# Kernel tuning notes

Hardware: AMD Instinct MI355X
Metric: run time of the kernel (lower is better)

Reference implementation:

```python
import jax, jax.numpy as jnp
import numpy as np

EPS = 0.001  # numerical_stabilizer


def setup_inputs() -> dict:
    key = jax.random.key(0)
    ks = jax.random.split(key, 8)
    B, L, D, H, M = 4, 4096, 1024, 16, 64
    scale = 0.02
    return {
        "query": jax.random.normal(ks[0], (B, L, D), jnp.float32),
        "key": jax.random.normal(ks[1], (B, L, D), jnp.float32),
        "value": jax.random.normal(ks[2], (B, L, D), jnp.float32),
        "Wq": jax.random.normal(ks[3], (D, H, M), jnp.float32) * scale,
        "bq": jnp.zeros((H, M), jnp.float32),
        "Wk": jax.random.normal(ks[4], (D, H, M), jnp.float32) * scale,
        "bk": jnp.zeros((H, M), jnp.float32),
        "Wv": jax.random.normal(ks[5], (D, H, M), jnp.float32) * scale,
        "bv": jnp.zeros((H, M), jnp.float32),
        "Wo": jax.random.normal(ks[6], (H, M, D), jnp.float32) * scale,
        "bo": jnp.zeros((D,), jnp.float32),
        "step": 0,
    }


def reference(query, key, value, Wq, bq, Wk, bk, Wv, bv, Wo, bo, step):
    # QKV projections: [B,L,D] x [D,H,M] -> [B,L,H,M]
    q = jnp.einsum('bld,dhm->blhm', query, Wq) + bq
    k = jnp.einsum('bld,dhm->blhm', key, Wk) + bk
    v = jnp.einsum('bld,dhm->blhm', value, Wv) + bv
    # ReLU feature map with stabilizer
    q = jax.nn.relu(q) + EPS
    k = jax.nn.relu(k) + EPS
    # Linear (kernelized) attention: KV outer-product state [B,H,M,M]
    kvs = jnp.einsum('blhm,blhd->bhmd', k, v)
    a_v = jnp.einsum('blhm,bhmd->blhd', q, kvs)
    # Normalizer: sum of keys over sequence
    ks_sum = jnp.sum(k, axis=1)                       # [B,H,M]
    norm = jnp.einsum('blhm,bhm->blh', q, ks_sum)     # [B,L,H]
    a_v = a_v / norm[..., None]
    # Output projection over (head, head_dim) -> hidden
    out = jnp.einsum('blhm,hmd->bld', a_v, Wo) + bo
    return out
```

## Files before the change

kernel.cpp:

```cpp
#include <hip/hip_runtime.h>
#include <stdint.h>


typedef __bf16 bf16;
typedef __bf16 bf16x4 __attribute__((ext_vector_type(4)));
typedef __bf16 bf16x8 __attribute__((ext_vector_type(8)));
typedef float f32x4 __attribute__((ext_vector_type(4)));

#define MFMA_(a, b, c) __builtin_amdgcn_mfma_f32_16x16x32_bf16((a), (b), (c), 0, 0, 0)

static constexpr int BB   = 4;
static constexpr int LSEQ = 4096;
static constexpr int DIM  = 1024;
static constexpr int HH   = 16;
static constexpr float EPSF = 0.001f;

__device__ __forceinline__ void gload16(bf16* lds, const bf16* g) {
  __builtin_amdgcn_global_load_lds(
      (const __attribute__((address_space(1))) void*)g,
      (__attribute__((address_space(3))) void*)lds, 16, 0, 0);
}

__global__ void k_cvt(const float* __restrict__ q, const float* __restrict__ k,
                      const float* __restrict__ v, bf16* __restrict__ xb) {
  const int nchunk = 3 << 21;
  const int stride = gridDim.x * blockDim.x;
  for (int c = blockIdx.x * blockDim.x + threadIdx.x; c < nchunk; c += stride) {
    const int t = c >> 21;
    const size_t off = (size_t)(c & ((1 << 21) - 1)) * 8;
    const float* src = (t == 0) ? q : (t == 1) ? k : v;
    const f32x4* sp = reinterpret_cast<const f32x4*>(src + off);
    const f32x4 a = __builtin_nontemporal_load(sp);
    const f32x4 b = __builtin_nontemporal_load(sp + 1);
    bf16x8 o;
    o[0] = (bf16)a[0]; o[1] = (bf16)a[1]; o[2] = (bf16)a[2]; o[3] = (bf16)a[3];
    o[4] = (bf16)b[0]; o[5] = (bf16)b[1]; o[6] = (bf16)b[2]; o[7] = (bf16)b[3];
    *reinterpret_cast<bf16x8*>(xb + (size_t)t * 16777216u + off) = o;
  }
}

__global__ void k_prep_w4(const float* __restrict__ W0, const float* __restrict__ W1,
                          const float* __restrict__ W2, const float* __restrict__ W3,
                          bf16* __restrict__ T0, bf16* __restrict__ T1,
                          bf16* __restrict__ T2, bf16* __restrict__ T3) {
  const float* W; bf16* T;
  switch (blockIdx.z) {
    case 0:  W = W0; T = T0; break;
    case 1:  W = W1; T = T1; break;
    case 2:  W = W2; T = T2; break;
    default: W = W3; T = T3; break;
  }
  __shared__ float t[32][33];
  const int tx = threadIdx.x & 31, ty = threadIdx.x >> 5;
  const int r0 = blockIdx.x * 32, c0 = blockIdx.y * 32;
#pragma unroll
  for (int j = 0; j < 32; j += 8)
    t[ty + j][tx] = W[(size_t)(r0 + ty + j) * DIM + c0 + tx];
  __syncthreads();
#pragma unroll
  for (int j = 0; j < 32; j += 8)
    T[(size_t)(c0 + ty + j) * DIM + r0 + tx] = (bf16)t[tx][ty + j];
}

__global__ void k_init_vt(bf16* __restrict__ vt) {
  const int c = blockIdx.x * 256 + threadIdx.x;
  const int l8 = c & 511;
  const int r  = (c >> 9) & 15;
  const int bh = c >> 13;
  const bf16 val = (r == 0) ? (bf16)1.0f : (bf16)0.0f;
  bf16x8 o;
#pragma unroll
  for (int j = 0; j < 8; ++j) o[j] = val;
  *reinterpret_cast<bf16x8*>(vt + ((size_t)bh * 80 + 64 + r) * LSEQ + l8 * 8) = o;
}

__device__ __forceinline__ void stage_half(bf16 (&As)[2][16384], bf16 (&Bs)[2][16384],
                                           const bf16* Ab, const bf16* Bb,
                                           int h, int w, int srow, int scol) {
  const int t = h >> 2, reg = h & 3, buf = t & 1;
  bf16* lds = (reg < 2) ? &As[buf][(reg & 1) * 8192] : &Bs[buf][(reg & 1) * 8192];
  const bf16* g = (reg < 2) ? Ab : Bb;
  const int rbase = (reg & 1) * 128;
#pragma unroll
  for (int rr = 0; rr < 2; ++rr) {
    const int row = rbase + (rr * 8 + w) * 8 + srow;
    gload16(lds + (rr * 8 + w) * 512, g + (size_t)row * DIM + t * 64 + scol);
  }
}

#define LDA(d, g, f)                                                                              \
  a[d][0] = *reinterpret_cast<const bf16x8*>(&As[g][(wm * 128 + (f) * 16 + lr) * 64 + col0]);     \
  a[d][1] = *reinterpret_cast<const bf16x8*>(&As[g][(wm * 128 + (f) * 16 + lr) * 64 + col1]);
#define LDB(d, g, c)                                                                              \
  b[d][0] = *reinterpret_cast<const bf16x8*>(&Bs[g][(wn * 64 + (c) * 16 + lr) * 64 + col0]);      \
  b[d][1] = *reinterpret_cast<const bf16x8*>(&Bs[g][(wn * 64 + (c) * 16 + lr) * 64 + col1]);
#define MM(fi, ci, fo, co)                                                                        \
  acc[fo][co] = MFMA_(a[fi][0], b[ci][0], acc[fo][co]);                                           \
  acc[fo][co] = MFMA_(a[fi][1], b[ci][1], acc[fo][co]);

#define PHASE(g, q, pidx)                                                                         \
  {                                                                                               \
    if ((q) == 0) { LDA(0, g, 0) LDA(1, g, 1) LDA(2, g, 2) LDA(3, g, 3)                           \
                    LDB(0, g, 0) LDB(1, g, 1) }                                                   \
    else if ((q) == 1) { LDB(0, g, 2) LDB(1, g, 3) }                                              \
    else if ((q) == 2) { LDA(0, g, 4) LDA(1, g, 5) LDA(2, g, 6) LDA(3, g, 7) }                    \
    else { LDB(0, g, 0) LDB(1, g, 1) }                                                            \
    const int hh = 8 * i + 5 + (pidx);                                                            \
    if (hh < 64) stage_half(As, Bs, Ab, Bb, hh, w, srow, scol);                                   \
    if ((pidx) == 3 || (pidx) == 7) {                                                             \
      if (i < 7) { asm volatile("s_waitcnt vmcnt(2)" ::: "memory"); }                             \
      else       { asm volatile("s_waitcnt vmcnt(0)" ::: "memory"); }                             \
    }                                                                                             \
    __builtin_amdgcn_sched_barrier(0);                                                            \
    __builtin_amdgcn_s_barrier();                                                                 \
    __builtin_amdgcn_sched_barrier(0);                                                            \
    __builtin_amdgcn_s_setprio(1);                                                                \
    if ((q) == 0) { MM(0, 0, 0, 0) MM(1, 0, 1, 0) MM(2, 0, 2, 0) MM(3, 0, 3, 0)                   \
                    MM(0, 1, 0, 1) MM(1, 1, 1, 1) MM(2, 1, 2, 1) MM(3, 1, 3, 1) }                 \
    else if ((q) == 1) { MM(0, 0, 0, 2) MM(1, 0, 1, 2) MM(2, 0, 2, 2) MM(3, 0, 3, 2)              \
                         MM(0, 1, 0, 3) MM(1, 1, 1, 3) MM(2, 1, 2, 3) MM(3, 1, 3, 3) }            \
    else if ((q) == 2) { MM(0, 0, 4, 2) MM(1, 0, 5, 2) MM(2, 0, 6, 2) MM(3, 0, 7, 2)              \
                         MM(0, 1, 4, 3) MM(1, 1, 5, 3) MM(2, 1, 6, 3) MM(3, 1, 7, 3) }            \
    else { MM(0, 0, 4, 0) MM(1, 0, 5, 0) MM(2, 0, 6, 0) MM(3, 0, 7, 0)                            \
           MM(0, 1, 4, 1) MM(1, 1, 5, 1) MM(2, 1, 6, 1) MM(3, 1, 7, 1) }                          \
    __builtin_amdgcn_s_setprio(0);                                                                \
    __builtin_amdgcn_sched_barrier(0);                                                            \
    __builtin_amdgcn_s_barrier();                                                                 \
    __builtin_amdgcn_sched_barrier(0);                                                            \
  }

template <int MODE>
__global__ __launch_bounds__(512, 2) void k_gemm256(const bf16* __restrict__ X,
                                                    const bf16* __restrict__ WT,
                                                    const float* __restrict__ bias,
                                                    void* __restrict__ outp) {
  __shared__ __align__(16) bf16 As[2][16384];
  __shared__ __align__(16) bf16 Bs[2][16384];
  const int tid = threadIdx.x;
  const int lane = tid & 63, w = tid >> 6;
  const int wm = w >> 2, wn = w & 3;
  const int lr = lane & 15, lk = (lane >> 4) & 3;
  const int n0 = blockIdx.x * 256, c0 = blockIdx.y * 256;
  const int swz = (lr & 7) * 8;
  const int col0 = (lk * 8) ^ swz;
  const int col1 = (lk * 8 + 32) ^ swz;
  const int srow = lane >> 3;
  const int scol = (((lane & 7) ^ ((lane >> 3) & 7)) * 8);
  const bf16* Ab = X + (size_t)n0 * DIM;
  const bf16* Bb = WT + (size_t)c0 * DIM;

  f32x4 acc[8][4] = {};
  bf16x8 a[4][2], b[2][2];

#pragma unroll
  for (int h = 0; h < 5; ++h) stage_half(As, Bs, Ab, Bb, h, w, srow, scol);
  asm volatile("s_waitcnt vmcnt(2)" ::: "memory");
  __builtin_amdgcn_sched_barrier(0);
  __builtin_amdgcn_s_barrier();
  __builtin_amdgcn_sched_barrier(0);

  for (int i = 0; i < 8; ++i) {
    PHASE(0, 0, 0) PHASE(0, 1, 1) PHASE(0, 2, 2) PHASE(0, 3, 3)
    PHASE(1, 0, 4) PHASE(1, 1, 5) PHASE(1, 2, 6) PHASE(1, 3, 7)
  }

  float bvv[4];
#pragma unroll
  for (int cb = 0; cb < 4; ++cb) bvv[cb] = bias[c0 + wn * 64 + cb * 16 + lr];
  const int bidx = n0 >> 12;
  const int l0 = n0 & (LSEQ - 1);
#pragma unroll
  for (int f = 0; f < 8; ++f) {
#pragma unroll
    for (int cb = 0; cb < 4; ++cb) {
      const int c = c0 + wn * 64 + cb * 16 + lr;
      if (MODE == 0) {
        bf16* out = (bf16*)outp;
#pragma unroll
        for (int r = 0; r < 4; ++r) {
          float x = acc[f][cb][r] + bvv[cb];
          x = fmaxf(x, 0.f) + EPSF;
          const int row = n0 + wm * 128 + f * 16 + lk * 4 + r;
          out[(size_t)row * DIM + c] = (bf16)x;
        }
      } else if (MODE == 3) {
        float* out = (float*)outp;
#pragma unroll
        for (int r = 0; r < 4; ++r) {
          const int row = n0 + wm * 128 + f * 16 + lk * 4 + r;
          out[(size_t)row * DIM + c] = acc[f][cb][r] + bvv[cb];
        }
      } else {
        bf16* out = (bf16*)outp;
        const int l = l0 + wm * 128 + f * 16 + lk * 4;
        bf16x4 o;
#pragma unroll
        for (int r = 0; r < 4; ++r) {
          float x = acc[f][cb][r] + bvv[cb];
          if (MODE == 1) x = fmaxf(x, 0.f) + EPSF;
          o[r] = (bf16)x;
        }
        size_t rowbase;
        if (MODE == 1) rowbase = (size_t)bidx * 1024 + c;
        else           rowbase = ((size_t)(bidx * HH + (c >> 6)) * 80 + (c & 63));
        *reinterpret_cast<bf16x4*>(out + rowbase * LSEQ + l) = o;
      }
    }
  }
}
#undef PHASE
#undef MM
#undef LDB
#undef LDA

__global__ __launch_bounds__(256, 2) void k_kvs(const bf16* __restrict__ kt,
                                                const bf16* __restrict__ vt,
                                                float* __restrict__ kvs) {
  const int tid = threadIdx.x, lane = tid & 63, wid = tid >> 6;
  const int lr = lane & 15, lk = lane >> 4;
  const int bh = blockIdx.y;
  const int lbase = blockIdx.x * 512;
  __shared__ bf16 As[64][64];
  __shared__ bf16 Bs[80][64];
  f32x4 acc[5] = {};
  const bf16* ktb = kt + (size_t)bh * 64 * LSEQ;
  const bf16* vtb = vt + (size_t)bh * 80 * LSEQ;

  for (int ks = 0; ks < 8; ++ks) {
    const int l0 = lbase + ks * 64;
    __syncthreads();
#pragma unroll
    for (int i = 0; i < 2; ++i) {
      const int e = i * 2048 + tid * 8;
      const int row = e >> 6, col = e & 63;
      *reinterpret_cast<bf16x8*>(&As[row][col]) =
          *reinterpret_cast<const bf16x8*>(ktb + (size_t)row * LSEQ + l0 + col);
    }
#pragma unroll
    for (int i = 0; i < 2; ++i) {
      const int e = i * 2048 + tid * 8;
      const int row = e >> 6, col = e & 63;
      *reinterpret_cast<bf16x8*>(&Bs[row][col]) =
          *reinterpret_cast<const bf16x8*>(vtb + (size_t)row * LSEQ + l0 + col);
    }
    if (tid < 128) {
      const int e = 4096 + tid * 8;
      const int row = e >> 6, col = e & 63;
      *reinterpret_cast<bf16x8*>(&Bs[row][col]) =
          *reinterpret_cast<const bf16x8*>(vtb + (size_t)row * LSEQ + l0 + col);
    }
    __syncthreads();
#pragma unroll
    for (int kk = 0; kk < 2; ++kk) {
      const bf16x8 af = *reinterpret_cast<const bf16x8*>(&As[wid * 16 + lr][kk * 32 + lk * 8]);
#pragma unroll
      for (int cb = 0; cb < 5; ++cb) {
        const bf16x8 bfr = *reinterpret_cast<const bf16x8*>(&Bs[cb * 16 + lr][kk * 32 + lk * 8]);
        acc[cb] = MFMA_(af, bfr, acc[cb]);
      }
    }
  }
  float* kb = kvs + (size_t)bh * 64 * 80;
#pragma unroll
  for (int cb = 0; cb < 5; ++cb) {
    const int dcol = cb * 16 + lr;
#pragma unroll
    for (int r = 0; r < 4; ++r) {
      const int m = wid * 16 + lk * 4 + r;
      atomicAdd(kb + m * 80 + dcol, acc[cb][r]);
    }
  }
}

__global__ void k_kvs_t(const float* __restrict__ kvs, bf16* __restrict__ bav) {
  const int bh = blockIdx.x;
  const float* src = kvs + (size_t)bh * 5120;
  bf16* dst = bav + (size_t)bh * 5120;
  for (int i = threadIdx.x; i < 5120; i += 256) {
    const int dp = i >> 6, mm = i & 63;
    dst[i] = (bf16)src[mm * 80 + dp];
  }
}

__global__ __launch_bounds__(256, 2) void k_av(const bf16* __restrict__ q,
                                               const bf16* __restrict__ bav,
                                               bf16* __restrict__ avn) {
  const int tid = threadIdx.x, lane = tid & 63, wid = tid >> 6;
  const int lr = lane & 15, lk = lane >> 4;
  const int bh = blockIdx.y, b = bh >> 4, h = bh & 15;
  const int l0 = blockIdx.x * 128;
  __shared__ bf16 As[128][64];
  __shared__ bf16 Bs[80][64];
  __shared__ float nrm[128];

  const bf16* qb = q + ((size_t)b * LSEQ + l0) * DIM + h * 64;
#pragma unroll
  for (int i = 0; i < 4; ++i) {
    const int e = i * 2048 + tid * 8;
    const int row = e >> 6, col = e & 63;
    *reinterpret_cast<bf16x8*>(&As[row][col]) =
        *reinterpret_cast<const bf16x8*>(qb + (size_t)row * DIM + col);
  }
  const bf16* bb = bav + (size_t)bh * 5120;
#pragma unroll
  for (int i = 0; i < 2; ++i) {
    const int e = i * 2048 + tid * 8;
    const int row = e >> 6, col = e & 63;
    *reinterpret_cast<bf16x8*>(&Bs[row][col]) =
        *reinterpret_cast<const bf16x8*>(bb + row * 64 + col);
  }
  if (tid < 128) {
    const int e = 4096 + tid * 8;
    const int row = e >> 6, col = e & 63;
    *reinterpret_cast<bf16x8*>(&Bs[row][col]) =
        *reinterpret_cast<const bf16x8*>(bb + row * 64 + col);
  }
  __syncthreads();

  f32x4 acc[2][5] = {};
#pragma unroll
  for (int kk = 0; kk < 2; ++kk) {
    bf16x8 af[2];
    af[0] = *reinterpret_cast<const bf16x8*>(&As[wid * 32 + lr][kk * 32 + lk * 8]);
    af[1] = *reinterpret_cast<const bf16x8*>(&As[wid * 32 + 16 + lr][kk * 32 + lk * 8]);
#pragma unroll
    for (int cb = 0; cb < 5; ++cb) {
      const bf16x8 bfr = *reinterpret_cast<const bf16x8*>(&Bs[cb * 16 + lr][kk * 32 + lk * 8]);
      acc[0][cb] = MFMA_(af[0], bfr, acc[0][cb]);
      acc[1][cb] = MFMA_(af[1], bfr, acc[1][cb]);
    }
  }
  if (lr == 0) {
#pragma unroll
    for (int rb = 0; rb < 2; ++rb)
#pragma unroll
      for (int r = 0; r < 4; ++r)
        nrm[wid * 32 + rb * 16 + lk * 4 + r] = acc[rb][4][r];
  }
  __syncthreads();
  bf16* ob = avn + ((size_t)b * LSEQ + l0) * DIM + h * 64;
#pragma unroll
  for (int rb = 0; rb < 2; ++rb) {
#pragma unroll
    for (int cb = 0; cb < 4; ++cb) {
#pragma unroll
      for (int r = 0; r < 4; ++r) {
        const int row = wid * 32 + rb * 16 + lk * 4 + r;
        const float x = acc[rb][cb][r] / nrm[row];
        ob[(size_t)row * DIM + cb * 16 + lr] = (bf16)x;
      }
    }
  }
}

extern "C" void kernel_launch(void* const* d_in, const int* in_sizes, int n_in,
                              void* d_out, int out_size, void* d_ws, size_t ws_size,
                              hipStream_t stream) {
  const float* query = (const float*)d_in[0];
  const float* key   = (const float*)d_in[1];
  const float* value = (const float*)d_in[2];
  const float* Wq    = (const float*)d_in[3];
  const float* bq    = (const float*)d_in[4];
  const float* Wk    = (const float*)d_in[5];
  const float* bk    = (const float*)d_in[6];
  const float* Wv    = (const float*)d_in[7];
  const float* bvp   = (const float*)d_in[8];
  const float* Wo    = (const float*)d_in[9];
  const float* bo    = (const float*)d_in[10];
  float* out = (float*)d_out;
  char* ws = (char*)d_ws;

  const size_t off_wqt = 0;
  const size_t off_wkt = off_wqt + (2u << 20);
  const size_t off_wvt = off_wkt + (2u << 20);
  const size_t off_wot = off_wvt + (2u << 20);
  const size_t off_xb  = off_wot + (2u << 20);
  const size_t off_vt  = off_xb  + 100663296ull;
  const size_t off_kvs = off_vt  + 41943040ull;
  const size_t off_bav = off_kvs + 1310720ull;
  const size_t total   = off_bav + 655360ull;
  if (ws_size < total) return;

  bf16*  WQT = (bf16*)(ws + off_wqt);
  bf16*  WKT = (bf16*)(ws + off_wkt);
  bf16*  WVT = (bf16*)(ws + off_wvt);
  bf16*  WOT = (bf16*)(ws + off_wot);
  bf16*  XB  = (bf16*)(ws + off_xb);
  bf16*  XBq = XB;
  bf16*  XBk = XB + 16777216u;
  bf16*  XBv = XB + 33554432u;
  bf16*  VT  = (bf16*)(ws + off_vt);
  float* KVS = (float*)(ws + off_kvs);
  bf16*  BAV = (bf16*)(ws + off_bav);
  bf16*  KT  = XBv;
  bf16*  Qb  = XBk;
  bf16*  AV  = XBq;

  k_cvt<<<2048, 256, 0, stream>>>(query, key, value, XB);
  k_prep_w4<<<dim3(32, 32, 4), 256, 0, stream>>>(Wq, Wk, Wv, Wo, WQT, WKT, WVT, WOT);
  k_init_vt<<<2048, 256, 0, stream>>>(VT);
  (void)hipMemsetAsync(KVS, 0, 1310720ull, stream);

  k_gemm256<2><<<dim3(64, 4), 512, 0, stream>>>(XBv, WVT, bvp, VT);
  k_gemm256<1><<<dim3(64, 4), 512, 0, stream>>>(XBk, WKT, bk, KT);
  k_gemm256<0><<<dim3(64, 4), 512, 0, stream>>>(XBq, WQT, bq, Qb);

  k_kvs<<<dim3(8, 64), 256, 0, stream>>>(KT, VT, KVS);
  k_kvs_t<<<64, 256, 0, stream>>>(KVS, BAV);

  k_av<<<dim3(32, 64), 256, 0, stream>>>(Qb, BAV, AV);

  k_gemm256<3><<<dim3(64, 4), 512, 0, stream>>>(AV, WOT, bo, out);
}
```

Measured before the change: 268.4 us.

## Stage GEMM epilogues through swizzled LDS for coalesced stores; split kvs finer

```diff
diff --git a/kernel.cpp b/kernel.cpp
--- a/kernel.cpp
+++ b/kernel.cpp
@@ -24,17 +24,36 @@
 __global__ void k_cvt(const float* __restrict__ q, const float* __restrict__ k,
                       const float* __restrict__ v, bf16* __restrict__ xb) {
   const int nchunk = 3 << 21;
-  const int stride = gridDim.x * blockDim.x;
-  for (int c = blockIdx.x * blockDim.x + threadIdx.x; c < nchunk; c += stride) {
+  const int nthr = gridDim.x * blockDim.x;
+  int c = blockIdx.x * blockDim.x + threadIdx.x;
+  for (; c + nthr < nchunk; c += 2 * nthr) {
+    const int c2 = c + nthr;
+    const int t1 = c >> 21, t2 = c2 >> 21;
+    const size_t o1 = (size_t)(c  & 0x1FFFFF) * 8;
+    const size_t o2 = (size_t)(c2 & 0x1FFFFF) * 8;
+    const float* s1 = (t1 == 0) ? q : (t1 == 1) ? k : v;
+    const float* s2 = (t2 == 0) ? q : (t2 == 1) ? k : v;
+    const f32x4 a0 = __builtin_nontemporal_load(reinterpret_cast<const f32x4*>(s1 + o1));
+    const f32x4 a1 = __builtin_nontemporal_load(reinterpret_cast<const f32x4*>(s1 + o1) + 1);
+    const f32x4 b0 = __builtin_nontemporal_load(reinterpret_cast<const f32x4*>(s2 + o2));
+    const f32x4 b1 = __builtin_nontemporal_load(reinterpret_cast<const f32x4*>(s2 + o2) + 1);
+    bf16x8 oa, ob;
+#pragma unroll
+    for (int j = 0; j < 4; ++j) { oa[j] = (bf16)a0[j]; oa[4 + j] = (bf16)a1[j]; }
+#pragma unroll
+    for (int j = 0; j < 4; ++j) { ob[j] = (bf16)b0[j]; ob[4 + j] = (bf16)b1[j]; }
+    *reinterpret_cast<bf16x8*>(xb + (size_t)t1 * 16777216u + o1) = oa;
+    *reinterpret_cast<bf16x8*>(xb + (size_t)t2 * 16777216u + o2) = ob;
+  }
+  if (c < nchunk) {
     const int t = c >> 21;
-    const size_t off = (size_t)(c & ((1 << 21) - 1)) * 8;
+    const size_t off = (size_t)(c & 0x1FFFFF) * 8;
     const float* src = (t == 0) ? q : (t == 1) ? k : v;
-    const f32x4* sp = reinterpret_cast<const f32x4*>(src + off);
-    const f32x4 a = __builtin_nontemporal_load(sp);
-    const f32x4 b = __builtin_nontemporal_load(sp + 1);
+    const f32x4 a = __builtin_nontemporal_load(reinterpret_cast<const f32x4*>(src + off));
+    const f32x4 b = __builtin_nontemporal_load(reinterpret_cast<const f32x4*>(src + off) + 1);
     bf16x8 o;
-    o[0] = (bf16)a[0]; o[1] = (bf16)a[1]; o[2] = (bf16)a[2]; o[3] = (bf16)a[3];
-    o[4] = (bf16)b[0]; o[5] = (bf16)b[1]; o[6] = (bf16)b[2]; o[7] = (bf16)b[3];
+#pragma unroll
+    for (int j = 0; j < 4; ++j) { o[j] = (bf16)a[j]; o[4 + j] = (bf16)b[j]; }
     *reinterpret_cast<bf16x8*>(xb + (size_t)t * 16777216u + off) = o;
   }
 }
@@ -74,11 +93,11 @@
   *reinterpret_cast<bf16x8*>(vt + ((size_t)bh * 80 + 64 + r) * LSEQ + l8 * 8) = o;
 }
 
-__device__ __forceinline__ void stage_half(bf16 (&As)[2][16384], bf16 (&Bs)[2][16384],
+__device__ __forceinline__ void stage_half(bf16* As0, bf16* Bs0,
                                            const bf16* Ab, const bf16* Bb,
                                            int h, int w, int srow, int scol) {
   const int t = h >> 2, reg = h & 3, buf = t & 1;
-  bf16* lds = (reg < 2) ? &As[buf][(reg & 1) * 8192] : &Bs[buf][(reg & 1) * 8192];
+  bf16* lds = ((reg < 2) ? As0 : Bs0) + buf * 16384 + (reg & 1) * 8192;
   const bf16* g = (reg < 2) ? Ab : Bb;
   const int rbase = (reg & 1) * 128;
 #pragma unroll
@@ -89,11 +108,11 @@
 }
 
 #define LDA(d, g, f)                                                                              \
-  a[d][0] = *reinterpret_cast<const bf16x8*>(&As[g][(wm * 128 + (f) * 16 + lr) * 64 + col0]);     \
-  a[d][1] = *reinterpret_cast<const bf16x8*>(&As[g][(wm * 128 + (f) * 16 + lr) * 64 + col1]);
+  a[d][0] = *reinterpret_cast<const bf16x8*>(&As0[(g) * 16384 + (wm * 128 + (f) * 16 + lr) * 64 + col0]); \
+  a[d][1] = *reinterpret_cast<const bf16x8*>(&As0[(g) * 16384 + (wm * 128 + (f) * 16 + lr) * 64 + col1]);
 #define LDB(d, g, c)                                                                              \
-  b[d][0] = *reinterpret_cast<const bf16x8*>(&Bs[g][(wn * 64 + (c) * 16 + lr) * 64 + col0]);      \
-  b[d][1] = *reinterpret_cast<const bf16x8*>(&Bs[g][(wn * 64 + (c) * 16 + lr) * 64 + col1]);
+  b[d][0] = *reinterpret_cast<const bf16x8*>(&Bs0[(g) * 16384 + (wn * 64 + (c) * 16 + lr) * 64 + col0]); \
+  b[d][1] = *reinterpret_cast<const bf16x8*>(&Bs0[(g) * 16384 + (wn * 64 + (c) * 16 + lr) * 64 + col1]);
 #define MM(fi, ci, fo, co)                                                                        \
   acc[fo][co] = MFMA_(a[fi][0], b[ci][0], acc[fo][co]);                                           \
   acc[fo][co] = MFMA_(a[fi][1], b[ci][1], acc[fo][co]);
@@ -106,7 +125,7 @@
     else if ((q) == 2) { LDA(0, g, 4) LDA(1, g, 5) LDA(2, g, 6) LDA(3, g, 7) }                    \
     else { LDB(0, g, 0) LDB(1, g, 1) }                                                            \
     const int hh = 8 * i + 5 + (pidx);                                                            \
-    if (hh < 64) stage_half(As, Bs, Ab, Bb, hh, w, srow, scol);                                   \
+    if (hh < 64) stage_half(As0, Bs0, Ab, Bb, hh, w, srow, scol);                                 \
     if ((pidx) == 3 || (pidx) == 7) {                                                             \
       if (i < 7) { asm volatile("s_waitcnt vmcnt(2)" ::: "memory"); }                             \
       else       { asm volatile("s_waitcnt vmcnt(0)" ::: "memory"); }                             \
@@ -134,8 +153,9 @@
                                                     const bf16* __restrict__ WT,
                                                     const float* __restrict__ bias,
                                                     void* __restrict__ outp) {
-  __shared__ __align__(16) bf16 As[2][16384];
-  __shared__ __align__(16) bf16 Bs[2][16384];
+  __shared__ __align__(16) bf16 SH[65536];
+  bf16* As0 = SH;
+  bf16* Bs0 = SH + 32768;
   const int tid = threadIdx.x;
   const int lane = tid & 63, w = tid >> 6;
   const int wm = w >> 2, wn = w & 3;
@@ -153,7 +173,7 @@
   bf16x8 a[4][2], b[2][2];
 
 #pragma unroll
-  for (int h = 0; h < 5; ++h) stage_half(As, Bs, Ab, Bb, h, w, srow, scol);
+  for (int h = 0; h < 5; ++h) stage_half(As0, Bs0, Ab, Bb, h, w, srow, scol);
   asm volatile("s_waitcnt vmcnt(2)" ::: "memory");
   __builtin_amdgcn_sched_barrier(0);
   __builtin_amdgcn_s_barrier();
@@ -169,30 +189,52 @@
   for (int cb = 0; cb < 4; ++cb) bvv[cb] = bias[c0 + wn * 64 + cb * 16 + lr];
   const int bidx = n0 >> 12;
   const int l0 = n0 & (LSEQ - 1);
-#pragma unroll
-  for (int f = 0; f < 8; ++f) {
-#pragma unroll
-    for (int cb = 0; cb < 4; ++cb) {
-      const int c = c0 + wn * 64 + cb * 16 + lr;
-      if (MODE == 0) {
-        bf16* out = (bf16*)outp;
-#pragma unroll
-        for (int r = 0; r < 4; ++r) {
-          float x = acc[f][cb][r] + bvv[cb];
-          x = fmaxf(x, 0.f) + EPSF;
-          const int row = n0 + wm * 128 + f * 16 + lk * 4 + r;
-          out[(size_t)row * DIM + c] = (bf16)x;
-        }
-      } else if (MODE == 3) {
-        float* out = (float*)outp;
+
+  if (MODE == 3) {
+    float* out = (float*)outp;
+#pragma unroll
+    for (int f = 0; f < 8; ++f)
+#pragma unroll
+      for (int cb = 0; cb < 4; ++cb) {
+        const int c = c0 + wn * 64 + cb * 16 + lr;
 #pragma unroll
         for (int r = 0; r < 4; ++r) {
           const int row = n0 + wm * 128 + f * 16 + lk * 4 + r;
           out[(size_t)row * DIM + c] = acc[f][cb][r] + bvv[cb];
         }
-      } else {
-        bf16* out = (bf16*)outp;
-        const int l = l0 + wm * 128 + f * 16 + lk * 4;
+      }
+  } else if (MODE == 0) {
+    __syncthreads();
+#pragma unroll
+    for (int f = 0; f < 8; ++f)
+#pragma unroll
+      for (int cb = 0; cb < 4; ++cb) {
+        const int cl = wn * 64 + cb * 16 + lr;
+#pragma unroll
+        for (int r = 0; r < 4; ++r) {
+          float x = acc[f][cb][r] + bvv[cb];
+          x = fmaxf(x, 0.f) + EPSF;
+          const int ll = wm * 128 + f * 16 + lk * 4 + r;
+          SH[ll * 256 + ((((cl >> 3) ^ (ll & 7)) << 3) | (cl & 7))] = (bf16)x;
+        }
+      }
+    __syncthreads();
+    bf16* outb = (bf16*)outp;
+#pragma unroll
+    for (int it = 0; it < 16; ++it) {
+      const int chunk = it * 512 + tid;
+      const int row = chunk >> 5, blk = chunk & 31;
+      const bf16x8 v = *reinterpret_cast<const bf16x8*>(&SH[row * 256 + ((blk ^ (row & 7)) << 3)]);
+      *reinterpret_cast<bf16x8*>(outb + (size_t)(n0 + row) * DIM + c0 + blk * 8) = v;
+    }
+  } else {
+    __syncthreads();
+#pragma unroll
+    for (int f = 0; f < 8; ++f)
+#pragma unroll
+      for (int cb = 0; cb < 4; ++cb) {
+        const int cl = wn * 64 + cb * 16 + lr;
+        const int ll = wm * 128 + f * 16 + lk * 4;
         bf16x4 o;
 #pragma unroll
         for (int r = 0; r < 4; ++r) {
@@ -200,11 +242,21 @@
           if (MODE == 1) x = fmaxf(x, 0.f) + EPSF;
           o[r] = (bf16)x;
         }
-        size_t rowbase;
-        if (MODE == 1) rowbase = (size_t)bidx * 1024 + c;
-        else           rowbase = ((size_t)(bidx * HH + (c >> 6)) * 80 + (c & 63));
-        *reinterpret_cast<bf16x4*>(out + rowbase * LSEQ + l) = o;
+        *reinterpret_cast<bf16x4*>(
+            &SH[cl * 256 + ((((ll >> 3) ^ (cl & 7)) << 3) | (ll & 7))]) = o;
       }
+    __syncthreads();
+    bf16* outb = (bf16*)outp;
+#pragma unroll
+    for (int it = 0; it < 16; ++it) {
+      const int chunk = it * 512 + tid;
+      const int row = chunk >> 5, blk = chunk & 31;
+      const bf16x8 v = *reinterpret_cast<const bf16x8*>(&SH[row * 256 + ((blk ^ (row & 7)) << 3)]);
+      const int cg = c0 + row;
+      size_t rowbase;
+      if (MODE == 1) rowbase = (size_t)bidx * 1024 + cg;
+      else           rowbase = ((size_t)(bidx * HH + (cg >> 6)) * 80 + (cg & 63));
+      *reinterpret_cast<bf16x8*>(outb + rowbase * LSEQ + l0 + blk * 8) = v;
     }
   }
 }
@@ -219,14 +271,14 @@
   const int tid = threadIdx.x, lane = tid & 63, wid = tid >> 6;
   const int lr = lane & 15, lk = lane >> 4;
   const int bh = blockIdx.y;
-  const int lbase = blockIdx.x * 512;
+  const int lbase = blockIdx.x * 256;
   __shared__ bf16 As[64][64];
   __shared__ bf16 Bs[80][64];
   f32x4 acc[5] = {};
   const bf16* ktb = kt + (size_t)bh * 64 * LSEQ;
   const bf16* vtb = vt + (size_t)bh * 80 * LSEQ;
 
-  for (int ks = 0; ks < 8; ++ks) {
+  for (int ks = 0; ks < 4; ++ks) {
     const int l0 = lbase + ks * 64;
     __syncthreads();
 #pragma unroll
@@ -405,7 +457,7 @@
   k_gemm256<1><<<dim3(64, 4), 512, 0, stream>>>(XBk, WKT, bk, KT);
   k_gemm256<0><<<dim3(64, 4), 512, 0, stream>>>(XBq, WQT, bq, Qb);
 
-  k_kvs<<<dim3(8, 64), 256, 0, stream>>>(KT, VT, KVS);
+  k_kvs<<<dim3(16, 64), 256, 0, stream>>>(KT, VT, KVS);
   k_kvs_t<<<64, 256, 0, stream>>>(KVS, BAV);
 
   k_av<<<dim3(32, 64), 256, 0, stream>>>(Qb, BAV, AV);
```

Result: faster. 256.8 us (-4.3%).
